# Kernel optimization log

Hardware: AMD Instinct MI355X
Metric: run time of the kernel (lower is better)

The kernel has to match this reference:

```python
import jax, jax.numpy as jnp
import numpy as np

B, H, W = 64, 14, 14
DIM, NH, LORA = 768, 12, 4
HD = DIM // NH  # 64


def setup_inputs() -> dict:
    key = jax.random.key(0)
    ks = jax.random.split(key, 12)
    s = 0.02
    return {
        "x": jax.random.normal(ks[0], (B, H, W, DIM), dtype=jnp.float32),
        "qkv_w": jax.random.normal(ks[1], (3 * DIM, DIM), dtype=jnp.float32) * s,
        "qkv_b": jax.random.normal(ks[2], (3 * DIM,), dtype=jnp.float32) * s,
        "proj_w": jax.random.normal(ks[3], (DIM, DIM), dtype=jnp.float32) * s,
        "proj_b": jax.random.normal(ks[4], (DIM,), dtype=jnp.float32) * s,
        "la_q": jax.random.normal(ks[5], (LORA, DIM), dtype=jnp.float32) * s,
        "lb_q": jax.random.normal(ks[6], (DIM, LORA), dtype=jnp.float32) * s,
        "la_v": jax.random.normal(ks[7], (LORA, DIM), dtype=jnp.float32) * s,
        "lb_v": jax.random.normal(ks[8], (DIM, LORA), dtype=jnp.float32) * s,
        "rel_pos_h": jax.random.normal(ks[9], (2 * H - 1, HD), dtype=jnp.float32) * s,
        "rel_pos_w": jax.random.normal(ks[10], (2 * W - 1, HD), dtype=jnp.float32) * s,
    }


def reference(x, qkv_w, qkv_b, proj_w, proj_b, la_q, lb_q, la_v, lb_v, rel_pos_h, rel_pos_w):
    b, h, w, c = x.shape
    nh, hd = NH, c // NH
    scale = hd ** -0.5

    # qkv projection with LoRA deltas on q and v
    qkv = x @ qkv_w.T + qkv_b                       # (b,h,w,3c)
    new_q = (x @ la_q.T) @ lb_q.T                   # (b,h,w,c)
    new_v = (x @ la_v.T) @ lb_v.T
    qkv = qkv.at[..., :c].add(new_q)
    qkv = qkv.at[..., 2 * c:].add(new_v)

    qkv = qkv.reshape(b, h * w, 3, nh, hd).transpose(2, 0, 3, 1, 4)
    qkv = qkv.reshape(3, b * nh, h * w, hd)
    q, k, v = qkv[0], qkv[1], qkv[2]

    attn = jnp.einsum('bqd,bkd->bqk', q * scale, k)  # (b*nh, hw, hw)

    # decomposed relative position bias; q_size == k_size so no interpolation
    idx_h = jnp.arange(h)[:, None] - jnp.arange(h)[None, :] + (h - 1)
    idx_w = jnp.arange(w)[:, None] - jnp.arange(w)[None, :] + (w - 1)
    Rh = rel_pos_h[idx_h]                            # (h,h,hd)
    Rw = rel_pos_w[idx_w]                            # (w,w,hd)
    r_q = q.reshape(b * nh, h, w, hd)
    rel_h = jnp.einsum('bhwc,hkc->bhwk', r_q, Rh)    # (b*nh,h,w,h)
    rel_w = jnp.einsum('bhwc,wkc->bhwk', r_q, Rw)    # (b*nh,h,w,w)
    attn = (attn.reshape(b * nh, h, w, h, w)
            + rel_h[:, :, :, :, None]
            + rel_w[:, :, :, None, :]).reshape(b * nh, h * w, h * w)

    attn = jax.nn.softmax(attn, axis=-1)
    out = jnp.einsum('bqk,bkd->bqd', attn, v)        # (b*nh, hw, hd)
    out = out.reshape(b, nh, h, w, hd).transpose(0, 2, 3, 1, 4).reshape(b, h, w, c)
    return out @ proj_w.T + proj_b
```

## Files before the change

### kernel.cpp

```cpp
#include <hip/hip_runtime.h>
#include <stdint.h>

#define DIM   768
#define NH    12
#define HD    64
#define NT    196
#define M_ROWS 12544

typedef __attribute__((ext_vector_type(8))) short bf16x8;
typedef __attribute__((ext_vector_type(4))) float f32x4;

__device__ __forceinline__ float b2f(short s) {
  union { unsigned u; float f; } c;
  c.u = ((unsigned)(unsigned short)s) << 16;
  return c.f;
}
__device__ __forceinline__ short f2b(float f) {
  union { float f; unsigned u; } c; c.f = f;
  unsigned u = c.u;
  u += 0x7fffu + ((u >> 16) & 1u);
  return (short)(u >> 16);
}

__device__ __forceinline__ f32x4 mfma16(bf16x8 a, bf16x8 b, f32x4 c) {
  return __builtin_amdgcn_mfma_f32_16x16x32_bf16(a, b, c, 0, 0, 0);
}

__device__ __forceinline__ void g2lds16(const short* g, short* l) {
  __builtin_amdgcn_global_load_lds(
      (const __attribute__((address_space(1))) void*)g,
      (__attribute__((address_space(3))) void*)l, 16, 0, 0);
}

struct CvtArgs { const float* src[4]; int n4[4]; int off[4]; };

__global__ __launch_bounds__(256) void k_cvt(CvtArgs a, short* __restrict__ dst) {
  const int tid = blockIdx.x * 256 + threadIdx.x;
  const int stride = gridDim.x * 256;
  #pragma unroll
  for (int s = 0; s < 4; ++s) {
    const float4* sp = (const float4*)a.src[s];
    short4* dp = (short4*)(dst + a.off[s]);
    const int n4 = a.n4[s];
    for (int i = tid; i < n4; i += stride) {
      float4 v = sp[i];
      short4 o = { f2b(v.x), f2b(v.y), f2b(v.z), f2b(v.w) };
      dp[i] = o;
    }
  }
}

__global__ __launch_bounds__(256) void k_lora_xa(
    const float* __restrict__ x, const float* __restrict__ la_q,
    const float* __restrict__ la_v, float* __restrict__ xa,
    short* __restrict__ xb)
{
  __shared__ float sla[8][DIM];
  const int tid = threadIdx.x;
  for (int i = tid; i < 8 * DIM; i += 256) {
    int j = i / DIM, c = i - j * DIM;
    sla[j][c] = (j < 4) ? la_q[j * DIM + c] : la_v[(j - 4) * DIM + c];
  }
  __syncthreads();
  const int lane = tid & 63, wid = tid >> 6;
  const int m = blockIdx.x * 4 + wid;
  const float4* xr = (const float4*)(x + (size_t)m * DIM);
  short4* xbr = (short4*)(xb + (size_t)m * DIM);
  float s[8] = {};
  #pragma unroll
  for (int i = 0; i < 3; ++i) {
    float4 xv = xr[lane + 64 * i];
    short4 o = { f2b(xv.x), f2b(xv.y), f2b(xv.z), f2b(xv.w) };
    xbr[lane + 64 * i] = o;
    int c = (lane + 64 * i) * 4;
    #pragma unroll
    for (int j = 0; j < 8; ++j)
      s[j] += xv.x * sla[j][c] + xv.y * sla[j][c + 1]
            + xv.z * sla[j][c + 2] + xv.w * sla[j][c + 3];
  }
  #pragma unroll
  for (int j = 0; j < 8; ++j) {
    #pragma unroll
    for (int off = 32; off; off >>= 1) s[j] += __shfl_xor(s[j], off);
  }
  if (lane == 0) {
    float* o = xa + m * 8;
    #pragma unroll
    for (int j = 0; j < 8; ++j) o[j] = s[j];
  }
}

template<int EPI, int NCOL>
__global__ __launch_bounds__(256) void k_gemm(
    const short* __restrict__ A, const short* __restrict__ B,
    const float* __restrict__ bias, const float* __restrict__ xa,
    const float* __restrict__ lb_q, const float* __restrict__ lb_v,
    short* __restrict__ out, float* __restrict__ outf)
{
  constexpr int K = DIM;
  constexpr int NWG = 98 * NCOL;
  constexpr int Q = NWG / 8, R = NWG % 8;
  __shared__ short sA[4096];
  __shared__ short sB[4096];

  const int g = blockIdx.x;
  const int xcd = g & 7, idx = g >> 3;
  const int wgid = (xcd < R) ? xcd * (Q + 1) + idx
                             : R * (Q + 1) + (xcd - R) * Q + idx;
  const int rm0 = (wgid / NCOL) * 128;
  const int cn0 = (wgid % NCOL) * 128;

  const int tid = threadIdx.x, lane = tid & 63, wid = tid >> 6;
  const int wm = (wid >> 1) * 64, wn = (wid & 1) * 64;
  const int fr = lane & 15, fg = lane >> 4;
  f32x4 acc[4][4] = {};

  const int r_ = tid >> 2;
  const int s_ = (tid & 3) ^ ((tid >> 3) & 3);
  const short* ga = A + (size_t)(rm0 + r_) * K + s_ * 8;
  const short* gb = B + (size_t)(cn0 + r_) * K + s_ * 8;
  short* lA = sA + wid * 512;
  short* lB = sB + wid * 512;
  const int swz8 = (fg ^ ((fr >> 1) & 3)) * 8;

  for (int kt = 0; kt < K; kt += 32) {
    g2lds16(ga + kt, lA);
    g2lds16(ga + 64 * K + kt, lA + 2048);
    g2lds16(gb + kt, lB);
    g2lds16(gb + 64 * K + kt, lB + 2048);
    __syncthreads();
    bf16x8 af[4], bg[4];
    #pragma unroll
    for (int i = 0; i < 4; ++i)
      af[i] = *(const bf16x8*)&sA[(wm + i * 16 + fr) * 32 + swz8];
    #pragma unroll
    for (int j = 0; j < 4; ++j)
      bg[j] = *(const bf16x8*)&sB[(wn + j * 16 + fr) * 32 + swz8];
    #pragma unroll
    for (int i = 0; i < 4; ++i)
      #pragma unroll
      for (int j = 0; j < 4; ++j)
        acc[i][j] = mfma16(af[i], bg[j], acc[i][j]);
    __syncthreads();
  }

  int ncol[4]; float biasv[4];
  #pragma unroll
  for (int j = 0; j < 4; ++j) {
    ncol[j] = cn0 + wn + j * 16 + fr;
    biasv[j] = bias[ncol[j]];
  }

  if (EPI == 0) {
    const int reg = cn0 / DIM;
    float lb[4][4];
    if (reg != 1) {
      const float* lbt = (reg == 0) ? lb_q : lb_v;
      #pragma unroll
      for (int j = 0; j < 4; ++j) {
        int ni = ncol[j] - reg * DIM;
        #pragma unroll
        for (int l = 0; l < 4; ++l) lb[j][l] = lbt[ni * 4 + l];
      }
    }
    #pragma unroll
    for (int i = 0; i < 4; ++i) {
      #pragma unroll
      for (int r = 0; r < 4; ++r) {
        int m = rm0 + wm + i * 16 + fg * 4 + r;
        int b_i = m / NT, p = m - b_i * NT;
        float xv0 = 0, xv1 = 0, xv2 = 0, xv3 = 0;
        if (reg != 1) {
          const float* xp = xa + m * 8 + (reg == 2 ? 4 : 0);
          xv0 = xp[0]; xv1 = xp[1]; xv2 = xp[2]; xv3 = xp[3];
        }
        #pragma unroll
        for (int j = 0; j < 4; ++j) {
          float val = acc[i][j][r] + biasv[j];
          if (reg != 1)
            val += xv0 * lb[j][0] + xv1 * lb[j][1] + xv2 * lb[j][2] + xv3 * lb[j][3];
          int ni = ncol[j] - reg * DIM;
          int head = ni >> 6, d = ni & 63;
          out[(size_t)reg * (M_ROWS * DIM)
              + ((size_t)(b_i * NH + head) * NT + p) * HD + d] = f2b(val);
        }
      }
    }
  } else {
    #pragma unroll
    for (int i = 0; i < 4; ++i)
      #pragma unroll
      for (int r = 0; r < 4; ++r) {
        int m = rm0 + wm + i * 16 + fg * 4 + r;
        #pragma unroll
        for (int j = 0; j < 4; ++j)
          outf[(size_t)m * DIM + ncol[j]] = acc[i][j][r] + biasv[j];
      }
  }
}

__global__ __launch_bounds__(256) void k_attn(
    const short* __restrict__ qb, const short* __restrict__ kb,
    const short* __restrict__ vb, const short* __restrict__ rph,
    const short* __restrict__ rpw, short* __restrict__ ao)
{
  __shared__ short vst[64][216];
  __shared__ short kst[NT * 64];
  __shared__ short pwb[4][16][120];
  __shared__ short relh[NT * 14];
  __shared__ short relw[NT * 14];
  const int tid = threadIdx.x, lane = tid & 63, wid = tid >> 6;
  const int fr = lane & 15, fg = lane >> 4;
  const int bh = blockIdx.x;
  const int b_i = bh / NH, head = bh - b_i * NH;
  const short* q0 = qb + (size_t)bh * NT * HD;
  const short* k0 = kb + (size_t)bh * NT * HD;
  const short* v0 = vb + (size_t)bh * NT * HD;

  for (int t = tid; t < NT * 8; t += 256) {
    int row = t >> 3, slot = t & 7;
    g2lds16(k0 + row * 64 + ((slot ^ (row & 7)) * 8), &kst[t * 8]);
  }

  for (int i = tid; i < 64 * 20; i += 256) {
    int d = i / 20, c = 196 + (i - (i / 20) * 20);
    vst[d][c] = 0;
  }
  for (int t = tid; t < NT * 8; t += 256) {
    int p = t >> 3, d0 = (t & 7) * 8;
    bf16x8 vv = *(const bf16x8*)(v0 + p * HD + d0);
    #pragma unroll
    for (int j = 0; j < 8; ++j) vst[d0 + j][p] = vv[j];
  }
  for (int job = wid; job < 28; job += 4) {
    const int isW = job >= 14 ? 1 : 0;
    const int fx = isW ? job - 14 : job;
    const int qrow = isW ? fr * 14 + fx : fx * 14 + fr;
    const bool aok = fr < 14;
    const short* rp = isW ? rpw : rph;
    int ridx = fx - fr + 13;
    ridx = ridx < 0 ? 0 : (ridx > 26 ? 26 : ridx);
    f32x4 racc = {0.f, 0.f, 0.f, 0.f};
    #pragma unroll
    for (int ks = 0; ks < 2; ++ks) {
      bf16x8 afr = {0,0,0,0,0,0,0,0};
      if (aok) afr = *(const bf16x8*)(q0 + qrow * HD + ks * 32 + fg * 8);
      bf16x8 bfr = *(const bf16x8*)(rp + ridx * HD + ks * 32 + fg * 8);
      racc = mfma16(afr, bfr, racc);
    }
    #pragma unroll
    for (int r = 0; r < 4; ++r) {
      int rr = fg * 4 + r;
      if (rr < 14 && fr < 14) {
        int p = isW ? rr * 14 + fx : fx * 14 + rr;
        (isW ? relw : relh)[p * 14 + fr] = f2b(racc[r]);
      }
    }
  }
  __syncthreads();

  const float scale = 0.125f;
  const int p0 = fg ^ (fr & 7);
  const int p1 = (fg + 4) ^ (fr & 7);
  for (int t = wid; t < 13; t += 4) {
    const int m0 = t * 16;
    bf16x8 aq0 = {0,0,0,0,0,0,0,0}, aq1 = {0,0,0,0,0,0,0,0};
    {
      int arow = m0 + fr;
      if (arow < NT) {
        aq0 = *(const bf16x8*)(q0 + arow * HD + fg * 8);
        aq1 = *(const bf16x8*)(q0 + arow * HD + 32 + fg * 8);
      }
    }
    f32x4 sc[13] = {};
    #pragma unroll
    for (int ct = 0; ct < 13; ++ct) {
      int brow = ct * 16 + fr;
      bf16x8 bk0 = {0,0,0,0,0,0,0,0}, bk1 = {0,0,0,0,0,0,0,0};
      if (brow < NT) {
        bk0 = *(const bf16x8*)&kst[brow * 64 + p0 * 8];
        bk1 = *(const bf16x8*)&kst[brow * 64 + p1 * 8];
      }
      sc[ct] = mfma16(aq0, bk0, sc[ct]);
      sc[ct] = mfma16(aq1, bk1, sc[ct]);
    }
    float rmax[4] = {-1e30f, -1e30f, -1e30f, -1e30f};
    #pragma unroll
    for (int ct = 0; ct < 13; ++ct) {
      int kk = ct * 16 + fr;
      int kh = kk / 14, kw = kk - kh * 14;
      #pragma unroll
      for (int r = 0; r < 4; ++r) {
        int p = m0 + fg * 4 + r;
        float v;
        if (kk < NT && p < NT)
          v = sc[ct][r] * scale + b2f(relh[p * 14 + kh]) + b2f(relw[p * 14 + kw]);
        else
          v = -1e30f;
        sc[ct][r] = v;
        rmax[r] = fmaxf(rmax[r], v);
      }
    }
    #pragma unroll
    for (int r = 0; r < 4; ++r) {
      rmax[r] = fmaxf(rmax[r], __shfl_xor(rmax[r], 1));
      rmax[r] = fmaxf(rmax[r], __shfl_xor(rmax[r], 2));
      rmax[r] = fmaxf(rmax[r], __shfl_xor(rmax[r], 4));
      rmax[r] = fmaxf(rmax[r], __shfl_xor(rmax[r], 8));
    }
    float rsum[4] = {0.f, 0.f, 0.f, 0.f};
    #pragma unroll
    for (int ct = 0; ct < 13; ++ct)
      #pragma unroll
      for (int r = 0; r < 4; ++r) {
        float e = __expf(sc[ct][r] - rmax[r]);
        sc[ct][r] = e;
        rsum[r] += e;
      }
    #pragma unroll
    for (int r = 0; r < 4; ++r) {
      rsum[r] += __shfl_xor(rsum[r], 1);
      rsum[r] += __shfl_xor(rsum[r], 2);
      rsum[r] += __shfl_xor(rsum[r], 4);
      rsum[r] += __shfl_xor(rsum[r], 8);
    }

    f32x4 oacc[4] = {};
    #pragma unroll
    for (int ct = 0; ct < 7; ++ct)
      #pragma unroll
      for (int r = 0; r < 4; ++r)
        pwb[wid][fg * 4 + r][ct * 16 + fr] = f2b(sc[ct][r]);
    #pragma unroll
    for (int ks = 0; ks < 4; ++ks) {
      const bool hi = (ks == 3) && (fg >= 2);
      bf16x8 pa = {0,0,0,0,0,0,0,0};
      if (!hi) pa = *(const bf16x8*)&pwb[wid][fr][ks * 32 + fg * 8];
      #pragma unroll
      for (int dt = 0; dt < 4; ++dt) {
        bf16x8 vv = {0,0,0,0,0,0,0,0};
        if (!hi) vv = *(const bf16x8*)&vst[dt * 16 + fr][ks * 32 + fg * 8];
        oacc[dt] = mfma16(pa, vv, oacc[dt]);
      }
    }
    #pragma unroll
    for (int ct = 7; ct < 13; ++ct)
      #pragma unroll
      for (int r = 0; r < 4; ++r)
        pwb[wid][fg * 4 + r][(ct - 7) * 16 + fr] = f2b(sc[ct][r]);
    #pragma unroll
    for (int ks = 0; ks < 3; ++ks) {
      bf16x8 pa = *(const bf16x8*)&pwb[wid][fr][ks * 32 + fg * 8];
      #pragma unroll
      for (int dt = 0; dt < 4; ++dt) {
        bf16x8 vv = *(const bf16x8*)&vst[dt * 16 + fr][112 + ks * 32 + fg * 8];
        oacc[dt] = mfma16(pa, vv, oacc[dt]);
      }
    }
    #pragma unroll
    for (int r = 0; r < 4; ++r) {
      int p = m0 + fg * 4 + r;
      if (p < NT) {
        float inv = 1.0f / rsum[r];
        size_t base = ((size_t)(b_i * NT + p)) * DIM + head * HD;
        #pragma unroll
        for (int dt = 0; dt < 4; ++dt)
          ao[base + dt * 16 + fr] = f2b(oacc[dt][r] * inv);
      }
    }
  }
}

extern "C" void kernel_launch(void* const* d_in, const int* in_sizes, int n_in,
                              void* d_out, int out_size, void* d_ws, size_t ws_size,
                              hipStream_t stream) {
  const float *x = nullptr, *qkv_w = nullptr, *qkv_b = nullptr,
              *proj_w = nullptr, *proj_b = nullptr, *rph = nullptr,
              *rpw = nullptr;
  const float* c3072[4] = {nullptr, nullptr, nullptr, nullptr};
  int n3072 = 0, n1728 = 0;
  for (int i = 0; i < n_in; ++i) {
    const float* p = (const float*)d_in[i];
    switch (in_sizes[i]) {
      case 9633792: x = p; break;
      case 1769472: qkv_w = p; break;
      case 2304:    qkv_b = p; break;
      case 589824:  proj_w = p; break;
      case 768:     proj_b = p; break;
      case 3072:    if (n3072 < 4) c3072[n3072++] = p; break;
      case 1728:    { if (n1728 == 0) rph = p; else rpw = p; ++n1728; } break;
      default: break;
    }
  }
  const bool alpha = (n_in >= 1 && in_sizes[n_in - 1] == 9633792);
  const float* la_q = c3072[0];
  const float* lb_q = alpha ? c3072[2] : c3072[1];
  const float* la_v = alpha ? c3072[1] : c3072[2];
  const float* lb_v = c3072[3];

  float* out = (float*)d_out;

  char* ws = (char*)d_ws;
  float* xa   = (float*)ws;
  short* qkvb = (short*)(ws + 401408);
  short* q_   = qkvb;
  short* k_   = qkvb + (size_t)M_ROWS * DIM;
  short* v_   = qkvb + (size_t)2 * M_ROWS * DIM;
  short* cvt  = (short*)(ws + 401408 + 57802752);
  short* xb      = cvt;
  short* qkv_wb  = cvt + 9633792;
  short* proj_wb = cvt + 11403264;
  short* rphb    = cvt + 11993088;
  short* rpwb    = cvt + 11994816;
  short* ao = xb;

  CvtArgs ca;
  ca.src[0] = qkv_w;  ca.n4[0] = 1769472 / 4;  ca.off[0] = 9633792;
  ca.src[1] = proj_w; ca.n4[1] =  589824 / 4;  ca.off[1] = 11403264;
  ca.src[2] = rph;    ca.n4[2] =    1728 / 4;  ca.off[2] = 11993088;
  ca.src[3] = rpw;    ca.n4[3] =    1728 / 4;  ca.off[3] = 11994816;

  k_cvt<<<512, 256, 0, stream>>>(ca, cvt);
  k_lora_xa<<<3136, 256, 0, stream>>>(x, la_q, la_v, xa, xb);
  k_gemm<0, 18><<<98 * 18, 256, 0, stream>>>(xb, qkv_wb, qkv_b, xa, lb_q, lb_v,
                                             qkvb, nullptr);
  k_attn<<<768, 256, 0, stream>>>(q_, k_, v_, rphb, rpwb, ao);
  k_gemm<1, 6><<<98 * 6, 256, 0, stream>>>(ao, proj_wb, proj_b, nullptr, nullptr,
                                           nullptr, nullptr, out);
}
```

Measured before the change: 194.8 us.

## Rewrite GEMMs as 256x256-tile double-buffered kernels with 512 threads

Replaces the 128x128-tile, 256-thread GEMM with a 256x256-tile, 8-wave kernel. It uses 128 KB of dynamic LDS to double-buffer 64-wide K slices, prefetches the next slice while MFMAs run on the current one, and raises wave priority around the MFMA bursts. The goal is to hide global-to-LDS latency and improve data reuse per tile. The cost is fewer workgroups (441 and 147 on a large-CU device), which hurts load balance and occupancy. It also adds the extra hipFuncSetAttribute calls on every launch.

```diff
diff --git a/kernel.cpp b/kernel.cpp
--- a/kernel.cpp
+++ b/kernel.cpp
@@ -91,58 +91,84 @@
 }
 
 template<int EPI, int NCOL>
-__global__ __launch_bounds__(256) void k_gemm(
+__global__ __launch_bounds__(512) void k_gemm2(
     const short* __restrict__ A, const short* __restrict__ B,
     const float* __restrict__ bias, const float* __restrict__ xa,
     const float* __restrict__ lb_q, const float* __restrict__ lb_v,
     short* __restrict__ out, float* __restrict__ outf)
 {
   constexpr int K = DIM;
-  constexpr int NWG = 98 * NCOL;
-  constexpr int Q = NWG / 8, R = NWG % 8;
-  __shared__ short sA[4096];
-  __shared__ short sB[4096];
+  constexpr int NWG = 49 * NCOL;
+  constexpr int Qc = NWG / 8, Rc = NWG % 8;
+  extern __shared__ short smem[];
 
   const int g = blockIdx.x;
   const int xcd = g & 7, idx = g >> 3;
-  const int wgid = (xcd < R) ? xcd * (Q + 1) + idx
-                             : R * (Q + 1) + (xcd - R) * Q + idx;
-  const int rm0 = (wgid / NCOL) * 128;
-  const int cn0 = (wgid % NCOL) * 128;
+  const int wgid = (xcd < Rc) ? xcd * (Qc + 1) + idx
+                              : Rc * (Qc + 1) + (xcd - Rc) * Qc + idx;
+  const int rm0 = (wgid / NCOL) * 256;
+  const int cn0 = (wgid % NCOL) * 256;
 
   const int tid = threadIdx.x, lane = tid & 63, wid = tid >> 6;
-  const int wm = (wid >> 1) * 64, wn = (wid & 1) * 64;
+  const int wm = (wid >> 2) * 128, wn = (wid & 3) * 64;
   const int fr = lane & 15, fg = lane >> 4;
-  f32x4 acc[4][4] = {};
-
-  const int r_ = tid >> 2;
-  const int s_ = (tid & 3) ^ ((tid >> 3) & 3);
-  const short* ga = A + (size_t)(rm0 + r_) * K + s_ * 8;
-  const short* gb = B + (size_t)(cn0 + r_) * K + s_ * 8;
-  short* lA = sA + wid * 512;
-  short* lB = sB + wid * 512;
+  f32x4 acc[8][4] = {};
+
+  const int srow = tid >> 2;
+  const int spos = ((tid & 3) ^ ((tid >> 3) & 3)) * 8;
+  const short* gaT = A + (size_t)(rm0 + srow) * K + spos;
+  const short* gbT = B + (size_t)(cn0 + srow) * K + spos;
   const int swz8 = (fg ^ ((fr >> 1) & 3)) * 8;
 
-  for (int kt = 0; kt < K; kt += 32) {
-    g2lds16(ga + kt, lA);
-    g2lds16(ga + 64 * K + kt, lA + 2048);
-    g2lds16(gb + kt, lB);
-    g2lds16(gb + 64 * K + kt, lB + 2048);
-    __syncthreads();
-    bf16x8 af[4], bg[4];
-    #pragma unroll
-    for (int i = 0; i < 4; ++i)
-      af[i] = *(const bf16x8*)&sA[(wm + i * 16 + fr) * 32 + swz8];
-    #pragma unroll
-    for (int j = 0; j < 4; ++j)
-      bg[j] = *(const bf16x8*)&sB[(wn + j * 16 + fr) * 32 + swz8];
-    #pragma unroll
-    for (int i = 0; i < 4; ++i)
-      #pragma unroll
-      for (int j = 0; j < 4; ++j)
-        acc[i][j] = mfma16(af[i], bg[j], acc[i][j]);
-    __syncthreads();
-  }
+#define STG(buf, T, s)                                                      \
+  do {                                                                      \
+    const short* g0 = ((s) & 1) ? gbT : gaT;                                \
+    short* d0 = smem + (buf) * 32768 + ((s) & 1) * 16384                    \
+                + ((s) >> 1) * 8192 + tid * 8;                              \
+    g2lds16(g0 + (T) * 64 + ((s) >> 1) * 32, d0);                           \
+    g2lds16(g0 + (size_t)128 * K + (T) * 64 + ((s) >> 1) * 32, d0 + 4096);  \
+  } while (0)
+
+  STG(0, 0, 0); STG(0, 0, 1); STG(0, 0, 2); STG(0, 0, 3);
+  asm volatile("s_waitcnt vmcnt(0)" ::: "memory");
+  __builtin_amdgcn_s_barrier();
+  __builtin_amdgcn_sched_barrier(0);
+
+  bf16x8 af[8];
+  for (int T = 0; T < 12; ++T) {
+    const int b = T & 1;
+    const short* pA = smem + b * 32768;
+    const short* pB = pA + 16384;
+    #pragma unroll
+    for (int q = 0; q < 4; ++q) {
+      const int kh = q >> 1, jh = q & 1;
+      if (jh == 0) {
+        #pragma unroll
+        for (int i = 0; i < 8; ++i)
+          af[i] = *(const bf16x8*)&pA[kh * 8192 + (wm + i * 16 + fr) * 32 + swz8];
+      }
+      bf16x8 bg0 = *(const bf16x8*)&pB[kh * 8192 + (wn + (jh * 2 + 0) * 16 + fr) * 32 + swz8];
+      bf16x8 bg1 = *(const bf16x8*)&pB[kh * 8192 + (wn + (jh * 2 + 1) * 16 + fr) * 32 + swz8];
+      if (T + 1 < 12) {
+        STG(b ^ 1, T + 1, q);
+        asm volatile("s_waitcnt vmcnt(4)" ::: "memory");
+      } else {
+        asm volatile("s_waitcnt vmcnt(0)" ::: "memory");
+      }
+      __builtin_amdgcn_s_barrier();
+      asm volatile("s_waitcnt lgkmcnt(0)" ::: "memory");
+      __builtin_amdgcn_sched_barrier(0);
+      __builtin_amdgcn_s_setprio(1);
+      #pragma unroll
+      for (int i = 0; i < 8; ++i) {
+        acc[i][jh * 2 + 0] = mfma16(af[i], bg0, acc[i][jh * 2 + 0]);
+        acc[i][jh * 2 + 1] = mfma16(af[i], bg1, acc[i][jh * 2 + 1]);
+      }
+      __builtin_amdgcn_s_setprio(0);
+      __builtin_amdgcn_s_barrier();
+    }
+  }
+#undef STG
 
   int ncol[4]; float biasv[4];
   #pragma unroll
@@ -164,7 +190,7 @@
       }
     }
     #pragma unroll
-    for (int i = 0; i < 4; ++i) {
+    for (int i = 0; i < 8; ++i) {
       #pragma unroll
       for (int r = 0; r < 4; ++r) {
         int m = rm0 + wm + i * 16 + fg * 4 + r;
@@ -188,7 +214,7 @@
     }
   } else {
     #pragma unroll
-    for (int i = 0; i < 4; ++i)
+    for (int i = 0; i < 8; ++i)
       #pragma unroll
       for (int r = 0; r < 4; ++r) {
         int m = rm0 + wm + i * 16 + fg * 4 + r;
@@ -420,11 +446,16 @@
   ca.src[2] = rph;    ca.n4[2] =    1728 / 4;  ca.off[2] = 11993088;
   ca.src[3] = rpw;    ca.n4[3] =    1728 / 4;  ca.off[3] = 11994816;
 
+  hipFuncSetAttribute((const void*)k_gemm2<0, 9>,
+                      hipFuncAttributeMaxDynamicSharedMemorySize, 131072);
+  hipFuncSetAttribute((const void*)k_gemm2<1, 3>,
+                      hipFuncAttributeMaxDynamicSharedMemorySize, 131072);
+
   k_cvt<<<512, 256, 0, stream>>>(ca, cvt);
   k_lora_xa<<<3136, 256, 0, stream>>>(x, la_q, la_v, xa, xb);
-  k_gemm<0, 18><<<98 * 18, 256, 0, stream>>>(xb, qkv_wb, qkv_b, xa, lb_q, lb_v,
-                                             qkvb, nullptr);
+  k_gemm2<0, 9><<<441, 512, 131072, stream>>>(xb, qkv_wb, qkv_b, xa, lb_q,
+                                              lb_v, qkvb, nullptr);
   k_attn<<<768, 256, 0, stream>>>(q_, k_, v_, rphb, rpwb, ao);
-  k_gemm<1, 6><<<98 * 6, 256, 0, stream>>>(ao, proj_wb, proj_b, nullptr, nullptr,
-                                           nullptr, nullptr, out);
-}
+  k_gemm2<1, 3><<<147, 512, 131072, stream>>>(ao, proj_wb, proj_b, nullptr,
+                                              nullptr, nullptr, nullptr, out);
+}
```

Result: faster. 188.0 us (-3.5%).
